# Optimization experiments

Measured on AMD Instinct MI355X. Metric: run time of the kernel, lower is better.

## Reference

```python
import jax, jax.numpy as jnp
import numpy as np

NUM_GENES = 20000
NUM_CLASS = 32
BATCH_SIZE = 8
N = NUM_GENES * BATCH_SIZE      # 160_000 total nodes
E = 2_560_000                    # edges (avg degree 16)
K = 10
ALPHA = 0.1


def setup_inputs() -> dict:
    key = jax.random.key(0)
    ks = jax.random.split(key, 9)
    x = jax.random.normal(ks[0], (N, 1), dtype=jnp.float32)
    edge_index = jax.random.randint(ks[1], (2, E), 0, N, dtype=jnp.int32)
    batch = jnp.repeat(jnp.arange(BATCH_SIZE, dtype=jnp.int32), NUM_GENES)
    exp_emb_table = jax.random.normal(ks[2], (NUM_GENES, NUM_CLASS), dtype=jnp.float32) * 0.1
    exp_bias_table = jax.random.normal(ks[3], (NUM_GENES, 1), dtype=jnp.float32) * 0.1
    s = 1.0 / np.sqrt(NUM_CLASS)
    W1 = jax.random.uniform(ks[4], (NUM_CLASS, NUM_CLASS), jnp.float32, -s, s)
    b1 = jax.random.uniform(ks[5], (NUM_CLASS,), jnp.float32, -s, s)
    W2 = jax.random.uniform(ks[6], (NUM_CLASS, NUM_CLASS), jnp.float32, -s, s)
    b2 = jax.random.uniform(ks[7], (NUM_CLASS,), jnp.float32, -s, s)
    return {"x": x, "edge_index": edge_index, "batch": batch,
            "exp_emb_table": exp_emb_table, "exp_bias_table": exp_bias_table,
            "W1": W1, "b1": b1, "W2": W2, "b2": b2}


def reference(x, edge_index, batch, exp_emb_table, exp_bias_table, W1, b1, W2, b2):
    # node_index tiles 0..num_genes-1 for each graph in the batch
    node_index = jnp.tile(jnp.arange(NUM_GENES), BATCH_SIZE)        # [N]
    h = exp_emb_table[node_index] * x + exp_bias_table[node_index]  # [N, C]
    # dropout is identity in eval mode
    h = jax.nn.relu(h @ W1.T + b1)
    h = h @ W2.T + b2

    # APPNP: gcn_norm with self-loops, then k power-iteration steps
    loops = jnp.arange(N, dtype=edge_index.dtype)
    row = jnp.concatenate([edge_index[0], loops])  # source
    col = jnp.concatenate([edge_index[1], loops])  # target
    deg = jax.ops.segment_sum(jnp.ones_like(col, dtype=h.dtype), col, num_segments=N)
    dinv = jnp.where(deg > 0, jax.lax.rsqrt(deg), 0.0)
    norm = (dinv[row] * dinv[col])[:, None]        # [E+N, 1]

    h0 = h
    def step(carry, _):
        agg = jax.ops.segment_sum(carry[row] * norm, col, num_segments=N)
        return (1.0 - ALPHA) * agg + ALPHA * h0, None
    h, _ = jax.lax.scan(step, h, None, length=K)

    # global mean pool over graphs
    sums = jax.ops.segment_sum(h, batch, num_segments=BATCH_SIZE)
    counts = jax.ops.segment_sum(jnp.ones((N, 1), h.dtype), batch, num_segments=BATCH_SIZE)
    return sums / counts  # [BATCH_SIZE, NUM_CLASS]
```

## Files before the change

kernel.cpp:

```cpp
#include <hip/hip_runtime.h>

typedef unsigned int u32;
typedef unsigned short u16;

#define NPB 64
#define P1CHUNK 8192
#define SPB 16
#define OUT_CHUNK 640

__device__ inline float bf2f(u16 b) { return __uint_as_float(((u32)b) << 16); }
__device__ inline u16 f2bf(float f) {
    u32 u = __float_as_uint(f);
    return (u16)((u + 0x7fffu + ((u >> 16) & 1u)) >> 16);
}
__device__ inline u32 pack2(float a, float b) { return (u32)f2bf(a) | ((u32)f2bf(b) << 16); }

__global__ void k_zero_i(int* __restrict__ p, int n) {
    int i = blockIdx.x * 256 + threadIdx.x;
    if (i < n) p[i] = 0;
}

__global__ void k_deg(const int* __restrict__ col, int E, int* __restrict__ deg) {
    int stride = gridDim.x * blockDim.x;
    for (int e = blockIdx.x * blockDim.x + threadIdx.x; e < E; e += stride)
        atomicAdd(&deg[col[e]], 1);
}

__global__ void k_cnt(const int* __restrict__ row, int E,
                      int* __restrict__ bcnt, int nbuckets) {
    extern __shared__ int h[];
    for (int i = threadIdx.x; i < nbuckets; i += blockDim.x) h[i] = 0;
    __syncthreads();
    int stride = gridDim.x * blockDim.x;
    for (int e = blockIdx.x * blockDim.x + threadIdx.x; e < E; e += stride)
        atomicAdd(&h[row[e] >> 6], 1);
    __syncthreads();
    for (int i = threadIdx.x; i < nbuckets; i += blockDim.x) {
        int v = h[i];
        if (v) atomicAdd(&bcnt[i], v);
    }
}

__global__ void k_scanB(const int* __restrict__ bcnt, int nbuckets,
                        int* __restrict__ boff, int* __restrict__ bCur,
                        int* __restrict__ soff, int* __restrict__ sCur,
                        int* __restrict__ offsets, int N, int E, int nsup) {
    __shared__ int s[1024];
    __shared__ int carry;
    int t = threadIdx.x;
    if (t == 0) carry = 0;
    __syncthreads();
    for (int base = 0; base < nbuckets; base += 1024) {
        int i = base + t;
        int v = (i < nbuckets) ? bcnt[i] : 0;
        s[t] = v;
        __syncthreads();
        for (int off = 1; off < 1024; off <<= 1) {
            int tmp = (t >= off) ? s[t - off] : 0;
            __syncthreads();
            s[t] += tmp;
            __syncthreads();
        }
        int pos = s[t] - v + carry;
        if (i < nbuckets) {
            boff[i] = pos;
            bCur[i] = pos;
            if ((i & 63) == 0) { soff[i >> 6] = pos; sCur[i >> 6] = pos; }
        }
        __syncthreads();
        if (t == 1023) carry += s[1023];
        __syncthreads();
    }
    if (t == 0) { boff[nbuckets] = E; soff[nsup] = E; offsets[N] = E; }
}

__global__ __launch_bounds__(512) void k_p1(const int* __restrict__ ei, int E,
                                            int* __restrict__ sCur, u32* __restrict__ buf1) {
    __shared__ int cnt[64];
    __shared__ int cur[64];
    int c0 = blockIdx.x * P1CHUNK;
    int c1 = min(E, c0 + P1CHUNK);
    int t = threadIdx.x;
    if (t < 64) cnt[t] = 0;
    __syncthreads();
    for (int e = c0 + t; e < c1; e += 512)
        atomicAdd(&cnt[ei[e] >> 12], 1);
    __syncthreads();
    if (t < 64) {
        int c = cnt[t];
        cur[t] = (c > 0) ? atomicAdd(&sCur[t], c) : 0;
    }
    __syncthreads();
    for (int e = c0 + t; e < c1; e += 512) {
        int s = ei[e];
        int d = ei[E + e];
        int p = atomicAdd(&cur[s >> 12], 1);
        buf1[p] = (u32)(d & 0x3FFFF) | ((u32)(s & 4095) << 18);
    }
}

__global__ __launch_bounds__(256) void k_p2(const u32* __restrict__ buf1,
                                            const int* __restrict__ soff,
                                            int* __restrict__ bCur,
                                            u32* __restrict__ binned) {
    __shared__ int cnt[64];
    __shared__ int cur[64];
    int sb = blockIdx.x / SPB;
    int ch = blockIdx.x % SPB;
    int s0 = soff[sb], s1 = soff[sb + 1];
    int per = (s1 - s0 + SPB - 1) / SPB;
    int c0 = s0 + ch * per;
    int c1 = min(s1, c0 + per);
    int t = threadIdx.x;
    if (t < 64) cnt[t] = 0;
    __syncthreads();
    for (int e = c0 + t; e < c1; e += 256)
        atomicAdd(&cnt[(buf1[e] >> 24) & 63], 1);
    __syncthreads();
    if (t < 64) {
        int c = cnt[t];
        cur[t] = (c > 0) ? atomicAdd(&bCur[(sb << 6) + t], c) : 0;
    }
    __syncthreads();
    for (int e = c0 + t; e < c1; e += 256) {
        u32 v = buf1[e];
        int p = atomicAdd(&cur[(v >> 24) & 63], 1);
        binned[p] = v & 0x00FFFFFFu;
    }
}

__global__ __launch_bounds__(256) void k_sort(const u32* __restrict__ binned,
                                              const int* __restrict__ boff,
                                              int* __restrict__ offsets,
                                              int* __restrict__ dsts, int N) {
    __shared__ int cnt[64];
    __shared__ int off[64];
    int b = blockIdx.x;
    int s0 = boff[b], s1 = boff[b + 1];
    int t = threadIdx.x;
    if (t < 64) cnt[t] = 0;
    __syncthreads();
    for (int e = s0 + t; e < s1; e += 256)
        atomicAdd(&cnt[(binned[e] >> 18) & 63], 1);
    __syncthreads();
    if (t == 0) {
        int acc = s0;
        #pragma unroll
        for (int i = 0; i < 64; ++i) { off[i] = acc; acc += cnt[i]; }
    }
    __syncthreads();
    int vbase = b << 6;
    if (t < 64 && vbase + t < N) offsets[vbase + t] = off[t];
    __syncthreads();
    if (t < 64) cnt[t] = off[t];
    __syncthreads();
    for (int e = s0 + t; e < s1; e += 256) {
        u32 v = binned[e];
        int p = atomicAdd(&cnt[(v >> 18) & 63], 1);
        dsts[p] = (int)(v & 0x3FFFFu);
    }
}

__global__ void k_dinv(const int* __restrict__ deg, float* __restrict__ dinv,
                       float* __restrict__ a, float* __restrict__ rd, int N) {
    int i = blockIdx.x * 256 + threadIdx.x;
    if (i < N) {
        float d = (float)(deg[i] + 1);
        float dv = rsqrtf(d);
        dinv[i] = dv;
        a[i] = 0.9f * dv * dv;
        rd[i] = sqrtf(d);
    }
}

__global__ __launch_bounds__(256) void k_AW(const float* __restrict__ emb,
                                            const float* __restrict__ W1,
                                            float* __restrict__ A, int ngenes) {
    __shared__ float w1[32][33];
    __shared__ float eb[8][33];
    int t = threadIdx.x;
    int j = t & 31, gl = t >> 5;
    for (int i = t; i < 1024; i += 256) w1[i >> 5][i & 31] = W1[i];
    int g = blockIdx.x * 8 + gl;
    if (g < ngenes) eb[gl][j] = emb[g * 32 + j];
    __syncthreads();
    if (g < ngenes) {
        float acc = 0.f;
        #pragma unroll
        for (int c = 0; c < 32; ++c) acc = fmaf(eb[gl][c], w1[j][c], acc);
        A[(size_t)g * 32 + j] = acc;
    }
}

__global__ void k_s1(const float* __restrict__ W1, float* __restrict__ s1) {
    int j = threadIdx.x;
    if (j < 32) {
        float acc = 0.f;
        #pragma unroll
        for (int c = 0; c < 32; ++c) acc += W1[j * 32 + c];
        s1[j] = acc;
    }
}

__global__ __launch_bounds__(256) void k_h0(const float* __restrict__ x,
                                            const float* __restrict__ A,
                                            const float* __restrict__ bias,
                                            const float* __restrict__ s1,
                                            const float* __restrict__ b1,
                                            const float* __restrict__ W2,
                                            const float* __restrict__ b2,
                                            const float* __restrict__ dinv,
                                            uint4* __restrict__ h0,
                                            uint4* __restrict__ q0,
                                            float* __restrict__ out, int out_n,
                                            int N, int ngenes) {
    int node = blockIdx.x * 256 + threadIdx.x;
    if (blockIdx.x == 0 && threadIdx.x < out_n) out[threadIdx.x] = 0.f;
    if (node >= N) return;
    int g = node % ngenes;
    float xv = x[node];
    float bv = bias[g];
    const float4* Ar = (const float4*)(A + (size_t)g * 32);
    float r1[32];
    #pragma unroll
    for (int q = 0; q < 8; ++q) {
        float4 a4 = Ar[q];
        r1[q * 4 + 0] = fmaxf(fmaf(xv, a4.x, fmaf(bv, s1[q * 4 + 0], b1[q * 4 + 0])), 0.f);
        r1[q * 4 + 1] = fmaxf(fmaf(xv, a4.y, fmaf(bv, s1[q * 4 + 1], b1[q * 4 + 1])), 0.f);
        r1[q * 4 + 2] = fmaxf(fmaf(xv, a4.z, fmaf(bv, s1[q * 4 + 2], b1[q * 4 + 2])), 0.f);
        r1[q * 4 + 3] = fmaxf(fmaf(xv, a4.w, fmaf(bv, s1[q * 4 + 3], b1[q * 4 + 3])), 0.f);
    }
    u32 ow[16];
    #pragma unroll
    for (int i = 0; i < 32; i += 2) {
        float accA = b2[i];
        float accB = b2[i + 1];
        #pragma unroll
        for (int j2 = 0; j2 < 32; ++j2) {
            accA = fmaf(r1[j2], W2[i * 32 + j2], accA);
            accB = fmaf(r1[j2], W2[(i + 1) * 32 + j2], accB);
        }
        ow[i >> 1] = pack2(accA, accB);
    }
    #pragma unroll
    for (int q = 0; q < 4; ++q) {
        uint4 o;
        o.x = ow[q * 4 + 0];
        o.y = ow[q * 4 + 1];
        o.z = ow[q * 4 + 2];
        o.w = ow[q * 4 + 3];
        h0[(size_t)node * 4 + q] = o;
    }
    int gb = node / ngenes;
    u32 lo = (u32)f2bf(dinv[node]);
    u32 hi = lo << 16;
    uint4 qo;
    qo.x = (gb == 0) ? lo : (gb == 1) ? hi : 0u;
    qo.y = (gb == 2) ? lo : (gb == 3) ? hi : 0u;
    qo.z = (gb == 4) ? lo : (gb == 5) ? hi : 0u;
    qo.w = (gb == 6) ? lo : (gb == 7) ? hi : 0u;
    q0[node] = qo;
}

__global__ __launch_bounds__(256) void k_prop8(const uint4* __restrict__ qin,
                                               uint4* __restrict__ qout,
                                               const float* __restrict__ a,
                                               const float* __restrict__ dinv,
                                               const int* __restrict__ offsets,
                                               const int* __restrict__ dsts,
                                               int N, int ngenes) {
    int node = blockIdx.x * 256 + threadIdx.x;
    if (node >= N) return;
    int s0 = offsets[node];
    int s1 = offsets[node + 1];
    uint4 self = qin[node];
    float c0 = bf2f((u16)self.x), c1 = bf2f((u16)(self.x >> 16));
    float c2 = bf2f((u16)self.y), c3 = bf2f((u16)(self.y >> 16));
    float c4 = bf2f((u16)self.z), c5 = bf2f((u16)(self.z >> 16));
    float c6 = bf2f((u16)self.w), c7 = bf2f((u16)(self.w >> 16));
    int e = s0;
    for (; e + 4 <= s1; e += 4) {
        uint4 vA = qin[dsts[e]];
        uint4 vB = qin[dsts[e + 1]];
        uint4 vC = qin[dsts[e + 2]];
        uint4 vD = qin[dsts[e + 3]];
        c0 += bf2f((u16)vA.x) + bf2f((u16)vB.x) + bf2f((u16)vC.x) + bf2f((u16)vD.x);
        c1 += bf2f((u16)(vA.x >> 16)) + bf2f((u16)(vB.x >> 16)) + bf2f((u16)(vC.x >> 16)) + bf2f((u16)(vD.x >> 16));
        c2 += bf2f((u16)vA.y) + bf2f((u16)vB.y) + bf2f((u16)vC.y) + bf2f((u16)vD.y);
        c3 += bf2f((u16)(vA.y >> 16)) + bf2f((u16)(vB.y >> 16)) + bf2f((u16)(vC.y >> 16)) + bf2f((u16)(vD.y >> 16));
        c4 += bf2f((u16)vA.z) + bf2f((u16)vB.z) + bf2f((u16)vC.z) + bf2f((u16)vD.z);
        c5 += bf2f((u16)(vA.z >> 16)) + bf2f((u16)(vB.z >> 16)) + bf2f((u16)(vC.z >> 16)) + bf2f((u16)(vD.z >> 16));
        c6 += bf2f((u16)vA.w) + bf2f((u16)vB.w) + bf2f((u16)vC.w) + bf2f((u16)vD.w);
        c7 += bf2f((u16)(vA.w >> 16)) + bf2f((u16)(vB.w >> 16)) + bf2f((u16)(vC.w >> 16)) + bf2f((u16)(vD.w >> 16));
    }
    for (; e < s1; ++e) {
        uint4 v = qin[dsts[e]];
        c0 += bf2f((u16)v.x); c1 += bf2f((u16)(v.x >> 16));
        c2 += bf2f((u16)v.y); c3 += bf2f((u16)(v.y >> 16));
        c4 += bf2f((u16)v.z); c5 += bf2f((u16)(v.z >> 16));
        c6 += bf2f((u16)v.w); c7 += bf2f((u16)(v.w >> 16));
    }
    float av = a[node];
    float qi = 0.1f * dinv[node];
    int gb = node / ngenes;
    c0 = av * c0 + ((gb == 0) ? qi : 0.f);
    c1 = av * c1 + ((gb == 1) ? qi : 0.f);
    c2 = av * c2 + ((gb == 2) ? qi : 0.f);
    c3 = av * c3 + ((gb == 3) ? qi : 0.f);
    c4 = av * c4 + ((gb == 4) ? qi : 0.f);
    c5 = av * c5 + ((gb == 5) ? qi : 0.f);
    c6 = av * c6 + ((gb == 6) ? qi : 0.f);
    c7 = av * c7 + ((gb == 7) ? qi : 0.f);
    uint4 o;
    o.x = pack2(c0, c1);
    o.y = pack2(c2, c3);
    o.z = pack2(c4, c5);
    o.w = pack2(c6, c7);
    qout[node] = o;
}

__global__ __launch_bounds__(256) void k_out(const uint4* __restrict__ q,
                                             const u16* __restrict__ h0,
                                             const float* __restrict__ rd,
                                             float* __restrict__ out,
                                             int N, int ngenes) {
    __shared__ float wq[64][8];
    __shared__ u16 hs[64][32];
    int t = threadIdx.x;
    int b = t >> 5, c = t & 31;
    float acc = 0.f;
    int base = blockIdx.x * OUT_CHUNK;
    int lim = min(N, base + OUT_CHUNK);
    for (int v0 = base; v0 < lim; v0 += 64) {
        int nv = min(64, lim - v0);
        __syncthreads();
        int r = t >> 2, w4 = t & 3;
        if (r < nv) {
            *(uint4*)&hs[r][w4 * 8] = ((const uint4*)(h0 + (size_t)(v0 + r) * 32))[w4];
            u32 wv = ((const u32*)&q[v0 + r])[w4];
            float rdv = rd[v0 + r];
            wq[r][w4 * 2] = bf2f((u16)wv) * rdv;
            wq[r][w4 * 2 + 1] = bf2f((u16)(wv >> 16)) * rdv;
        }
        __syncthreads();
        for (int i = 0; i < nv; ++i)
            acc = fmaf(wq[i][b], bf2f(hs[i][c]), acc);
    }
    atomicAdd(&out[b * 32 + c], acc / (float)ngenes);
}

extern "C" void kernel_launch(void* const* d_in, const int* in_sizes, int n_in,
                              void* d_out, int out_size, void* d_ws, size_t ws_size,
                              hipStream_t stream) {
    const float* x    = (const float*)d_in[0];
    const int*   ei   = (const int*)d_in[1];
    const float* emb  = (const float*)d_in[3];
    const float* bias = (const float*)d_in[4];
    const float* W1   = (const float*)d_in[5];
    const float* b1   = (const float*)d_in[6];
    const float* W2   = (const float*)d_in[7];
    const float* b2   = (const float*)d_in[8];
    float* out = (float*)d_out;

    int N = in_sizes[0];
    int E = in_sizes[1] / 2;
    int ngenes = in_sizes[4];
    int nbuckets = (N + NPB - 1) / NPB;
    int nsup = (nbuckets + 63) / 64;

    char* pws = (char*)d_ws;
    auto carve = [&](size_t bytes) {
        void* r = (void*)pws;
        pws += (bytes + 255) & ~(size_t)255;
        return r;
    };
    u16*   h0      = (u16*)carve((size_t)N * 32 * 2);
    uint4* qA      = (uint4*)carve((size_t)N * 16);
    uint4* qB      = (uint4*)carve((size_t)N * 16);
    float* Amat    = (float*)carve((size_t)ngenes * 32 * 4);
    float* s1v     = (float*)carve(32 * 4);
    float* dinv    = (float*)carve((size_t)N * 4);
    float* afac    = (float*)carve((size_t)N * 4);
    float* rd      = (float*)carve((size_t)N * 4);
    int*   offsets = (int*)carve((size_t)(N + 1) * 4);
    int*   deg     = (int*)carve((size_t)N * 4);
    int*   bcnt    = (int*)carve((size_t)nbuckets * 4);
    int*   boff    = (int*)carve((size_t)(nbuckets + 1) * 4);
    int*   bCur    = (int*)carve((size_t)nbuckets * 4);
    int*   soff    = (int*)carve(65 * 4);
    int*   sCur    = (int*)carve(64 * 4);
    u32*   buf1    = (u32*)carve((size_t)E * 4);
    u32*   binned  = (u32*)carve((size_t)E * 4);
    int*   dsts    = (int*)carve((size_t)E * 4);

    int nbN = (N + 255) / 256;
    int zlen = (int)(bcnt - deg) + nbuckets;

    hipLaunchKernelGGL(k_zero_i, dim3((zlen + 255) / 256), dim3(256), 0, stream, deg, zlen);
    hipLaunchKernelGGL(k_cnt, dim3(160), dim3(256), nbuckets * 4, stream, ei, E, bcnt, nbuckets);
    hipLaunchKernelGGL(k_deg, dim3(2048), dim3(256), 0, stream, ei + E, E, deg);
    hipLaunchKernelGGL(k_scanB, dim3(1), dim3(1024), 0, stream,
                       bcnt, nbuckets, boff, bCur, soff, sCur, offsets, N, E, nsup);
    hipLaunchKernelGGL(k_p1, dim3((E + P1CHUNK - 1) / P1CHUNK), dim3(512), 0, stream,
                       ei, E, sCur, buf1);
    hipLaunchKernelGGL(k_dinv, dim3(nbN), dim3(256), 0, stream, deg, dinv, afac, rd, N);
    hipLaunchKernelGGL(k_p2, dim3(nsup * SPB), dim3(256), 0, stream, buf1, soff, bCur, binned);
    hipLaunchKernelGGL(k_sort, dim3(nbuckets), dim3(256), 0, stream,
                       binned, boff, offsets, dsts, N);
    hipLaunchKernelGGL(k_AW, dim3((ngenes + 7) / 8), dim3(256), 0, stream, emb, W1, Amat, ngenes);
    hipLaunchKernelGGL(k_s1, dim3(1), dim3(64), 0, stream, W1, s1v);
    hipLaunchKernelGGL(k_h0, dim3(nbN), dim3(256), 0, stream,
                       x, Amat, bias, s1v, b1, W2, b2, dinv,
                       (uint4*)h0, qA, out, out_size, N, ngenes);

    const uint4* qin = qA;
    for (int it = 0; it < 10; ++it) {
        uint4* qo = (it & 1) ? qA : qB;
        hipLaunchKernelGGL(k_prop8, dim3(nbN), dim3(256), 0, stream,
                           qin, qo, afac, dinv, offsets, dsts, N, ngenes);
        qin = qo;
    }

    hipLaunchKernelGGL(k_out, dim3((N + OUT_CHUNK - 1) / OUT_CHUNK), dim3(256), 0, stream,
                       qin, h0, rd, out, N, ngenes);
}
```

Measured before the change: 436.6 us.

## Compute in-degree via two-pass binning and shared-memory histograms instead of global atomics

Replaces the global-atomic degree count with a partition pass: destinations are bucketed into 4096-node super-bins (counted in k_cnt, scanned in k_scanB), scattered as 16-bit local indices, then histogrammed in shared memory per super-bin before a few global atomic adds. The aim is to remove 2.56M contended random global atomics. In exchange it adds two kernels, an extra E*2-byte buffer and an extra pass over the destination array.

```diff
diff --git a/kernel.cpp b/kernel.cpp
--- a/kernel.cpp
+++ b/kernel.cpp
@@ -5,7 +5,9 @@
 
 #define NPB 64
 #define P1CHUNK 8192
+#define DPCHUNK 8192
 #define SPB 16
+#define DHCHUNK 8
 #define OUT_CHUNK 640
 
 __device__ inline float bf2f(u16 b) { return __uint_as_float(((u32)b) << 16); }
@@ -20,31 +22,33 @@
     if (i < n) p[i] = 0;
 }
 
-__global__ void k_deg(const int* __restrict__ col, int E, int* __restrict__ deg) {
+__global__ void k_cnt(const int* __restrict__ ei, int E,
+                      int* __restrict__ bcnt, int* __restrict__ dscnt, int nbuckets) {
+    extern __shared__ int h[];
+    for (int i = threadIdx.x; i < nbuckets + 64; i += blockDim.x) h[i] = 0;
+    __syncthreads();
     int stride = gridDim.x * blockDim.x;
-    for (int e = blockIdx.x * blockDim.x + threadIdx.x; e < E; e += stride)
-        atomicAdd(&deg[col[e]], 1);
-}
-
-__global__ void k_cnt(const int* __restrict__ row, int E,
-                      int* __restrict__ bcnt, int nbuckets) {
-    extern __shared__ int h[];
-    for (int i = threadIdx.x; i < nbuckets; i += blockDim.x) h[i] = 0;
-    __syncthreads();
-    int stride = gridDim.x * blockDim.x;
-    for (int e = blockIdx.x * blockDim.x + threadIdx.x; e < E; e += stride)
-        atomicAdd(&h[row[e] >> 6], 1);
+    for (int e = blockIdx.x * blockDim.x + threadIdx.x; e < E; e += stride) {
+        atomicAdd(&h[ei[e] >> 6], 1);
+        atomicAdd(&h[nbuckets + (ei[E + e] >> 12)], 1);
+    }
     __syncthreads();
     for (int i = threadIdx.x; i < nbuckets; i += blockDim.x) {
         int v = h[i];
         if (v) atomicAdd(&bcnt[i], v);
     }
+    if (threadIdx.x < 64) {
+        int v = h[nbuckets + threadIdx.x];
+        if (v) atomicAdd(&dscnt[threadIdx.x], v);
+    }
 }
 
 __global__ void k_scanB(const int* __restrict__ bcnt, int nbuckets,
+                        const int* __restrict__ dscnt,
                         int* __restrict__ boff, int* __restrict__ bCur,
                         int* __restrict__ soff, int* __restrict__ sCur,
-                        int* __restrict__ offsets, int N, int E, int nsup) {
+                        int* __restrict__ dsoff, int* __restrict__ dsCur,
+                        int* __restrict__ offsets, int N, int E, int nsup, int nsupD) {
     __shared__ int s[1024];
     __shared__ int carry;
     int t = threadIdx.x;
@@ -71,7 +75,15 @@
         if (t == 1023) carry += s[1023];
         __syncthreads();
     }
-    if (t == 0) { boff[nbuckets] = E; soff[nsup] = E; offsets[N] = E; }
+    if (t == 0) {
+        boff[nbuckets] = E; soff[nsup] = E; offsets[N] = E;
+        int acc = 0;
+        for (int i = 0; i < nsupD; ++i) {
+            dsoff[i] = acc; dsCur[i] = acc;
+            acc += dscnt[i];
+        }
+        dsoff[nsupD] = E;
+    }
 }
 
 __global__ __launch_bounds__(512) void k_p1(const int* __restrict__ ei, int E,
@@ -96,6 +108,53 @@
         int d = ei[E + e];
         int p = atomicAdd(&cur[s >> 12], 1);
         buf1[p] = (u32)(d & 0x3FFFF) | ((u32)(s & 4095) << 18);
+    }
+}
+
+__global__ __launch_bounds__(256) void k_dp1(const int* __restrict__ col, int E,
+                                             int* __restrict__ dsCur, u16* __restrict__ dbuf) {
+    __shared__ int cnt[64];
+    __shared__ int cur[64];
+    int c0 = blockIdx.x * DPCHUNK;
+    int c1 = min(E, c0 + DPCHUNK);
+    int t = threadIdx.x;
+    if (t < 64) cnt[t] = 0;
+    __syncthreads();
+    for (int e = c0 + t; e < c1; e += 256)
+        atomicAdd(&cnt[col[e] >> 12], 1);
+    __syncthreads();
+    if (t < 64) {
+        int c = cnt[t];
+        cur[t] = (c > 0) ? atomicAdd(&dsCur[t], c) : 0;
+    }
+    __syncthreads();
+    for (int e = c0 + t; e < c1; e += 256) {
+        int d = col[e];
+        int p = atomicAdd(&cur[d >> 12], 1);
+        dbuf[p] = (u16)(d & 4095);
+    }
+}
+
+__global__ __launch_bounds__(256) void k_dhist(const u16* __restrict__ dbuf,
+                                               const int* __restrict__ dsoff,
+                                               int* __restrict__ deg, int N) {
+    __shared__ int h[4096];
+    int sup = blockIdx.x / DHCHUNK;
+    int ch = blockIdx.x % DHCHUNK;
+    int t = threadIdx.x;
+    for (int i = t; i < 4096; i += 256) h[i] = 0;
+    __syncthreads();
+    int s0 = dsoff[sup], s1 = dsoff[sup + 1];
+    int per = (s1 - s0 + DHCHUNK - 1) / DHCHUNK;
+    int c0 = s0 + ch * per;
+    int c1 = min(s1, c0 + per);
+    for (int e = c0 + t; e < c1; e += 256)
+        atomicAdd(&h[dbuf[e]], 1);
+    __syncthreads();
+    int vbase = sup << 12;
+    for (int i = t; i < 4096; i += 256) {
+        int v = h[i];
+        if (v && vbase + i < N) atomicAdd(&deg[vbase + i], v);
     }
 }
 
@@ -367,6 +426,7 @@
     int ngenes = in_sizes[4];
     int nbuckets = (N + NPB - 1) / NPB;
     int nsup = (nbuckets + 63) / 64;
+    int nsupD = (N + 4095) / 4096;
 
     char* pws = (char*)d_ws;
     auto carve = [&](size_t bytes) {
@@ -385,24 +445,33 @@
     int*   offsets = (int*)carve((size_t)(N + 1) * 4);
     int*   deg     = (int*)carve((size_t)N * 4);
     int*   bcnt    = (int*)carve((size_t)nbuckets * 4);
+    int*   dscnt   = (int*)carve(64 * 4);
     int*   boff    = (int*)carve((size_t)(nbuckets + 1) * 4);
     int*   bCur    = (int*)carve((size_t)nbuckets * 4);
     int*   soff    = (int*)carve(65 * 4);
     int*   sCur    = (int*)carve(64 * 4);
+    int*   dsoff   = (int*)carve(65 * 4);
+    int*   dsCur   = (int*)carve(64 * 4);
     u32*   buf1    = (u32*)carve((size_t)E * 4);
     u32*   binned  = (u32*)carve((size_t)E * 4);
     int*   dsts    = (int*)carve((size_t)E * 4);
+    u16*   dbuf    = (u16*)carve((size_t)E * 2);
 
     int nbN = (N + 255) / 256;
-    int zlen = (int)(bcnt - deg) + nbuckets;
+    int zlen = (int)(dscnt - deg) + 64;
 
     hipLaunchKernelGGL(k_zero_i, dim3((zlen + 255) / 256), dim3(256), 0, stream, deg, zlen);
-    hipLaunchKernelGGL(k_cnt, dim3(160), dim3(256), nbuckets * 4, stream, ei, E, bcnt, nbuckets);
-    hipLaunchKernelGGL(k_deg, dim3(2048), dim3(256), 0, stream, ei + E, E, deg);
+    hipLaunchKernelGGL(k_cnt, dim3(160), dim3(256), (nbuckets + 64) * 4, stream,
+                       ei, E, bcnt, dscnt, nbuckets);
     hipLaunchKernelGGL(k_scanB, dim3(1), dim3(1024), 0, stream,
-                       bcnt, nbuckets, boff, bCur, soff, sCur, offsets, N, E, nsup);
+                       bcnt, nbuckets, dscnt, boff, bCur, soff, sCur, dsoff, dsCur,
+                       offsets, N, E, nsup, nsupD);
     hipLaunchKernelGGL(k_p1, dim3((E + P1CHUNK - 1) / P1CHUNK), dim3(512), 0, stream,
                        ei, E, sCur, buf1);
+    hipLaunchKernelGGL(k_dp1, dim3((E + DPCHUNK - 1) / DPCHUNK), dim3(256), 0, stream,
+                       ei + E, E, dsCur, dbuf);
+    hipLaunchKernelGGL(k_dhist, dim3(nsupD * DHCHUNK), dim3(256), 0, stream,
+                       dbuf, dsoff, deg, N);
     hipLaunchKernelGGL(k_dinv, dim3(nbN), dim3(256), 0, stream, deg, dinv, afac, rd, N);
     hipLaunchKernelGGL(k_p2, dim3(nsup * SPB), dim3(256), 0, stream, buf1, soff, bCur, binned);
     hipLaunchKernelGGL(k_sort, dim3(nbuckets), dim3(256), 0, stream,
```

Result: faster. 386.0 us (-11.6%).
